# Kernel optimization log

Hardware: AMD Instinct MI355X
Metric: run time of the kernel (lower is better)

## Reference

```python
import jax, jax.numpy as jnp
import numpy as np
import math

WIDTH_POW = 10
WIDTH = 2 ** WIDTH_POW      # 1024
DEPTH = 20
BATCH = 8192
TWO_PI = 2.0 * math.pi


def setup_inputs() -> dict:
    key = jax.random.key(0)
    kx, ka = jax.random.split(key)
    # X is [width, batch] (features-first, matching the torch module's dim-0 padding)
    X = jax.random.normal(kx, (WIDTH, BATCH), dtype=jnp.float32)
    # angles ~ Uniform[0, 2*pi), as in the torch initializer
    angles = jax.random.uniform(ka, (DEPTH, WIDTH // 2), dtype=jnp.float32) * TWO_PI
    return {"X": X, "angles": angles}


def _butterfly_layer(X, ang, stride):
    # X: [width, batch]; ang: [width//2]
    w, b = X.shape
    # Pairs: within each block of 2*stride, element j rotates with element j+stride.
    Xr = X.reshape(w // (2 * stride), 2, stride, b)
    x0 = Xr[:, 0]  # [nblocks, stride, batch]
    x1 = Xr[:, 1]
    c = jnp.cos(ang).reshape(-1, stride, 1)
    s = jnp.sin(ang).reshape(-1, stride, 1)
    y0 = c * x0 + s * x1
    y1 = -s * x0 + c * x1
    return jnp.stack([y0, y1], axis=1).reshape(w, b)


def reference(X, angles):
    width = angles.shape[1] * 2
    width_pow = int(round(math.log2(width)))
    # Pad feature dim up to width (no-op here since X.shape[0] == width)
    pad = width - X.shape[0]
    if pad > 0:
        X = jnp.concatenate([X, jnp.zeros((pad, X.shape[1]), dtype=X.dtype)], axis=0)
    depth = angles.shape[0]
    for i in range(depth):  # small fixed loop over layers (structurally distinct strides)
        stride = 2 ** (i % width_pow)
        X = _butterfly_layer(X, angles[i], stride)
    return X
```

## Files before the change

kernel.cpp:

```cpp
#include <hip/hip_runtime.h>
#include <math.h>


#define NROW   1024
#define BATCH  8192
#define BATCH2 (BATCH / 2)
#define DEPTH  20
#define NANG   512
#define TAB_ELEMS (DEPTH * NANG)
#define TAB_BYTES ((size_t)TAB_ELEMS * 8)

typedef float v2f __attribute__((ext_vector_type(2)));

__device__ __host__ __forceinline__ int rowA(int sub, int i){ return (sub << 5) | i; }
__device__ __host__ __forceinline__ int rowB(int sub, int i){ return sub | (i << 5); }

__global__ void build_tab_kernel(const float* __restrict__ ang,
                                 float2* __restrict__ tab) {
    int idx = blockIdx.x * blockDim.x + threadIdx.x;
    if (idx >= TAB_ELEMS) return;
    int l = idx >> 9;
    int slot = idx & (NANG - 1);
    int sub = slot >> 4, p = slot & 15;
    int m10 = l % 10;
    int sp = m10;
    int SL = 1 << (m10 % 5);
    int i0 = 2 * (p / SL) * SL + p % SL;
    int r = (m10 >= 5) ? rowB(sub, i0) : rowA(sub, i0);
    int a = ((r >> (sp + 1)) << sp) | (r & ((1 << sp) - 1));
    float th = ang[l * NANG + a];
    float sv, cv;
    sincosf(th, &sv, &cv);
    tab[idx] = make_float2(cv, sv);
}

__device__ __forceinline__ void rotp(v2f& a, v2f& b, float cv, float sv) {
    v2f c = {cv, cv}, s = {sv, sv};
    v2f x0 = a, x1 = b;
    a = __builtin_elementwise_fma(c, x0, s * x1);
    b = __builtin_elementwise_fma(-s, x0, c * x1);
}

template<int SL>
__device__ __forceinline__ void layer_tab(v2f y[32],
                                          const float4* __restrict__ q4) {
    #pragma unroll
    for (int v = 0; v < 8; ++v) {
        float4 q = q4[v];
        int p0 = 2 * v, p1 = 2 * v + 1;
        int a0 = 2 * (p0 / SL) * SL + p0 % SL;
        int a1 = 2 * (p1 / SL) * SL + p1 % SL;
        rotp(y[a0], y[a0 + SL], q.x, q.y);
        rotp(y[a1], y[a1 + SL], q.z, q.w);
    }
}

template<int SL, bool PB, int SP>
__device__ __forceinline__ void layer_notab(v2f y[32],
                                            const float* __restrict__ angL,
                                            int sub) {
    #pragma unroll
    for (int p = 0; p < 16; ++p) {
        int i0 = 2 * (p / SL) * SL + p % SL;
        int r = PB ? rowB(sub, i0) : rowA(sub, i0);
        int a = ((r >> (SP + 1)) << SP) | (r & ((1 << SP) - 1));
        float th = angL[a];
        float sv, cv;
        __sincosf(th, &sv, &cv);
        rotp(y[i0], y[i0 + SL], cv, sv);
    }
}

template<bool USE_TAB>
__global__ __launch_bounds__(256) void butterfly_kernel(
        const float* __restrict__ X, const float* __restrict__ ang,
        const float2* __restrict__ tab, float* __restrict__ out) {
    __shared__ v2f lds[8 * 1024];
    int t = threadIdx.x;
    int c = t & 7;
    int sub = t >> 3;
    int bid = blockIdx.x;
    int L = ((bid & 7) << 6) | (bid >> 3);
    int col2 = (L << 3) + c;
    int xr = (c & 7) << 1;
    v2f* base = lds + (c << 10);

    v2f y[32];
    const v2f* Xp = reinterpret_cast<const v2f*>(X) + col2;
    #pragma unroll
    for (int i = 0; i < 32; ++i)
        y[i] = Xp[rowA(sub, i) * BATCH2];

    const float4* tf4 = reinterpret_cast<const float4*>(tab);
    if (USE_TAB) {
        layer_tab<1 >(y, tf4 + 0 * 256 + 8 * sub);
        layer_tab<2 >(y, tf4 + 1 * 256 + 8 * sub);
        layer_tab<4 >(y, tf4 + 2 * 256 + 8 * sub);
        layer_tab<8 >(y, tf4 + 3 * 256 + 8 * sub);
        layer_tab<16>(y, tf4 + 4 * 256 + 8 * sub);
    } else {
        layer_notab<1 ,false,0>(y, ang + 0 * NANG, sub);
        layer_notab<2 ,false,1>(y, ang + 1 * NANG, sub);
        layer_notab<4 ,false,2>(y, ang + 2 * NANG, sub);
        layer_notab<8 ,false,3>(y, ang + 3 * NANG, sub);
        layer_notab<16,false,4>(y, ang + 4 * NANG, sub);
    }
    #pragma unroll
    for (int u = 0; u < 16; ++u)
        *reinterpret_cast<float4*>(&base[((sub << 5) + 2 * u) ^ xr]) =
            make_float4(y[2*u].x, y[2*u].y, y[2*u+1].x, y[2*u+1].y);
    __syncthreads();
    #pragma unroll
    for (int i = 0; i < 32; ++i) y[i] = base[rowB(sub, i) ^ xr];

    if (USE_TAB) {
        layer_tab<1 >(y, tf4 + 5 * 256 + 8 * sub);
        layer_tab<2 >(y, tf4 + 6 * 256 + 8 * sub);
        layer_tab<4 >(y, tf4 + 7 * 256 + 8 * sub);
        layer_tab<8 >(y, tf4 + 8 * 256 + 8 * sub);
        layer_tab<16>(y, tf4 + 9 * 256 + 8 * sub);
    } else {
        layer_notab<1 ,true,5>(y, ang + 5 * NANG, sub);
        layer_notab<2 ,true,6>(y, ang + 6 * NANG, sub);
        layer_notab<4 ,true,7>(y, ang + 7 * NANG, sub);
        layer_notab<8 ,true,8>(y, ang + 8 * NANG, sub);
        layer_notab<16,true,9>(y, ang + 9 * NANG, sub);
    }
    __syncthreads();
    #pragma unroll
    for (int i = 0; i < 32; ++i) base[rowB(sub, i) ^ xr] = y[i];
    __syncthreads();
    #pragma unroll
    for (int u = 0; u < 16; ++u) {
        float4 v = *reinterpret_cast<const float4*>(&base[((sub << 5) + 2 * u) ^ xr]);
        y[2*u].x = v.x; y[2*u].y = v.y; y[2*u+1].x = v.z; y[2*u+1].y = v.w;
    }

    if (USE_TAB) {
        layer_tab<1 >(y, tf4 + 10 * 256 + 8 * sub);
        layer_tab<2 >(y, tf4 + 11 * 256 + 8 * sub);
        layer_tab<4 >(y, tf4 + 12 * 256 + 8 * sub);
        layer_tab<8 >(y, tf4 + 13 * 256 + 8 * sub);
        layer_tab<16>(y, tf4 + 14 * 256 + 8 * sub);
    } else {
        layer_notab<1 ,false,0>(y, ang + 10 * NANG, sub);
        layer_notab<2 ,false,1>(y, ang + 11 * NANG, sub);
        layer_notab<4 ,false,2>(y, ang + 12 * NANG, sub);
        layer_notab<8 ,false,3>(y, ang + 13 * NANG, sub);
        layer_notab<16,false,4>(y, ang + 14 * NANG, sub);
    }
    __syncthreads();
    #pragma unroll
    for (int u = 0; u < 16; ++u)
        *reinterpret_cast<float4*>(&base[((sub << 5) + 2 * u) ^ xr]) =
            make_float4(y[2*u].x, y[2*u].y, y[2*u+1].x, y[2*u+1].y);
    __syncthreads();
    #pragma unroll
    for (int i = 0; i < 32; ++i) y[i] = base[rowB(sub, i) ^ xr];

    if (USE_TAB) {
        layer_tab<1 >(y, tf4 + 15 * 256 + 8 * sub);
        layer_tab<2 >(y, tf4 + 16 * 256 + 8 * sub);
        layer_tab<4 >(y, tf4 + 17 * 256 + 8 * sub);
        layer_tab<8 >(y, tf4 + 18 * 256 + 8 * sub);
        layer_tab<16>(y, tf4 + 19 * 256 + 8 * sub);
    } else {
        layer_notab<1 ,true,5>(y, ang + 15 * NANG, sub);
        layer_notab<2 ,true,6>(y, ang + 16 * NANG, sub);
        layer_notab<4 ,true,7>(y, ang + 17 * NANG, sub);
        layer_notab<8 ,true,8>(y, ang + 18 * NANG, sub);
        layer_notab<16,true,9>(y, ang + 19 * NANG, sub);
    }

    v2f* Op = reinterpret_cast<v2f*>(out) + col2;
    #pragma unroll
    for (int i = 0; i < 32; ++i)
        Op[rowB(sub, i) * BATCH2] = y[i];
}

extern "C" void kernel_launch(void* const* d_in, const int* in_sizes, int n_in,
                              void* d_out, int out_size, void* d_ws, size_t ws_size,
                              hipStream_t stream) {
    (void)in_sizes; (void)n_in; (void)out_size;
    const float* X   = (const float*)d_in[0];
    const float* ang = (const float*)d_in[1];
    float* out = (float*)d_out;

    bool use_tab = (d_ws != nullptr) && (ws_size >= TAB_BYTES);
    if (use_tab) {
        float2* tab = (float2*)d_ws;
        build_tab_kernel<<<(TAB_ELEMS + 255) / 256, 256, 0, stream>>>(ang, tab);
        butterfly_kernel<true><<<512, 256, 0, stream>>>(X, ang, tab, out);
    } else {
        butterfly_kernel<false><<<512, 256, 0, stream>>>(X, ang, nullptr, out);
    }
}
```

Before: 31.60 us.

## Fuse butterfly layer groups into dense 32x32 matrices applied via bf16 MFMA

Each group of five butterfly layers, which acts inside 32-row subspaces, is folded into a dense 32x32 rotation matrix per subspace. The matrices are built in a preprocessing kernel and split into bf16 hi/lo parts. The main kernel applies the four group matrices with bf16 MFMA instructions, keeping intermediates in LDS between groups. The activations X and the intermediate results are rounded to bf16 at every stage, so precision drops well below the fp32 reference, and MFMA matrix products replace the VALU rotation arithmetic.

```diff
diff --git a/kernel.cpp b/kernel.cpp
--- a/kernel.cpp
+++ b/kernel.cpp
@@ -9,8 +9,146 @@
 #define NANG   512
 #define TAB_ELEMS (DEPTH * NANG)
 #define TAB_BYTES ((size_t)TAB_ELEMS * 8)
+#define WS_MFMA_BYTES ((size_t)(4 * 32 * 1024) * 2 * 2)
 
 typedef float v2f __attribute__((ext_vector_type(2)));
+using bf16x8 = __attribute__((ext_vector_type(8))) short;
+using f32x4  = __attribute__((ext_vector_type(4))) float;
+
+__device__ __forceinline__ unsigned short f2b(float f) {
+    union { float f; unsigned int u; } v; v.f = f;
+    unsigned int u = v.u;
+    return (unsigned short)((u + 0x7FFFu + ((u >> 16) & 1u)) >> 16);
+}
+__device__ __forceinline__ float b2f(unsigned short b) {
+    union { unsigned int u; float f; } v; v.u = ((unsigned int)b) << 16;
+    return v.f;
+}
+
+__global__ void build_w_kernel(const float* __restrict__ ang,
+                               unsigned short* __restrict__ whi,
+                               unsigned short* __restrict__ wlo) {
+    int idx = blockIdx.x * blockDim.x + threadIdx.x;
+    if (idx >= 4096) return;
+    int grp = idx >> 10, b = (idx >> 5) & 31, j = idx & 31;
+    float v[32];
+    #pragma unroll
+    for (int i = 0; i < 32; ++i) v[i] = (i == j) ? 1.f : 0.f;
+    #pragma unroll
+    for (int q = 0; q < 5; ++q) {
+        int SL = 1 << q;
+        int sp = (grp & 1) ? q + 5 : q;
+        int l  = grp * 5 + q;
+        int s  = 1 << sp;
+        #pragma unroll
+        for (int p = 0; p < 16; ++p) {
+            int i0 = ((p >> q) << (q + 1)) | (p & (SL - 1));
+            int i1 = i0 + SL;
+            int r0 = (grp & 1) ? ((i0 << 5) | b) : ((b << 5) | i0);
+            int a  = ((r0 >> (sp + 1)) << sp) | (r0 & (s - 1));
+            float th = ang[l * NANG + a];
+            float sv, cv; sincosf(th, &sv, &cv);
+            float x0 = v[i0], x1 = v[i1];
+            v[i0] = cv * x0 + sv * x1;
+            v[i1] = cv * x1 - sv * x0;
+        }
+    }
+    int mat = grp * 32 + b;
+    #pragma unroll
+    for (int i = 0; i < 32; ++i) {
+        unsigned short h = f2b(v[i]);
+        whi[mat * 1024 + i * 32 + j] = h;
+        wlo[mat * 1024 + i * 32 + j] = f2b(v[i] - b2f(h));
+    }
+}
+
+__global__ __launch_bounds__(512) void mfma_kernel(
+        const float* __restrict__ X,
+        const unsigned short* __restrict__ whi,
+        const unsigned short* __restrict__ wlo,
+        float* __restrict__ out) {
+    __shared__ __align__(16) unsigned short sbuf[2][32768];
+    int t  = threadIdx.x;
+    int ln = t & 63;
+    int w  = t >> 6;
+    int bid = blockIdx.x;
+    int L = ((bid & 7) << 5) | (bid >> 3);
+    int col0 = L << 5;
+
+    {
+        int cc = t & 15, sg = (t >> 4) & 1, bb = t >> 5;
+        int col = col0 + sg * 16 + cc;
+        #pragma unroll
+        for (int half = 0; half < 2; ++half) {
+            int rb = bb + 16 * half;
+            int site = rb * 2 + sg;
+            #pragma unroll
+            for (int g = 0; g < 4; ++g) {
+                unsigned int uu[4];
+                #pragma unroll
+                for (int jj = 0; jj < 4; ++jj) {
+                    float va = X[(rb * 32 + g * 8 + 2 * jj) * BATCH + col];
+                    float vb = X[(rb * 32 + g * 8 + 2 * jj + 1) * BATCH + col];
+                    uu[jj] = (unsigned int)f2b(va) | ((unsigned int)f2b(vb) << 16);
+                }
+                *reinterpret_cast<uint4*>(&sbuf[0][site * 512 + g * 128 + cc * 8]) =
+                    make_uint4(uu[0], uu[1], uu[2], uu[3]);
+            }
+        }
+    }
+    __syncthreads();
+
+    const bf16x8* WH = reinterpret_cast<const bf16x8*>(whi);
+    const bf16x8* WL = reinterpret_cast<const bf16x8*>(wlo);
+    int r15 = ln & 15, kg = ln >> 4;
+
+    #pragma unroll
+    for (int grp = 0; grp < 4; ++grp) {
+        int cur = grp & 1;
+        #pragma unroll
+        for (int m = 0; m < 4; ++m) {
+            int rb  = (w & 7) + 8 * m;
+            int mat = grp * 32 + rb;
+            bf16x8 ah0 = WH[mat * 128 + (r15     ) * 4 + kg];
+            bf16x8 ah1 = WH[mat * 128 + (r15 + 16) * 4 + kg];
+            bf16x8 al0 = WL[mat * 128 + (r15     ) * 4 + kg];
+            bf16x8 al1 = WL[mat * 128 + (r15 + 16) * 4 + kg];
+            #pragma unroll
+            for (int sg2 = 0; sg2 < 2; ++sg2) {
+                int site = rb * 2 + sg2;
+                bf16x8 bf = *reinterpret_cast<const bf16x8*>(
+                    &sbuf[cur][site * 512 + kg * 128 + r15 * 8]);
+                f32x4 acc0 = {0.f, 0.f, 0.f, 0.f};
+                f32x4 acc1 = {0.f, 0.f, 0.f, 0.f};
+                acc0 = __builtin_amdgcn_mfma_f32_16x16x32_bf16(ah0, bf, acc0, 0, 0, 0);
+                acc0 = __builtin_amdgcn_mfma_f32_16x16x32_bf16(al0, bf, acc0, 0, 0, 0);
+                acc1 = __builtin_amdgcn_mfma_f32_16x16x32_bf16(ah1, bf, acc1, 0, 0, 0);
+                acc1 = __builtin_amdgcn_mfma_f32_16x16x32_bf16(al1, bf, acc1, 0, 0, 0);
+                if (grp < 3) {
+                    #pragma unroll
+                    for (int e = 0; e < 4; ++e) {
+                        int k0 = kg * 4 + e;
+                        int k1 = 16 + kg * 4 + e;
+                        sbuf[cur ^ 1][(k0 * 2 + sg2) * 512 + (rb >> 3) * 128 +
+                                      r15 * 8 + (rb & 7)] = f2b(acc0[e]);
+                        sbuf[cur ^ 1][(k1 * 2 + sg2) * 512 + (rb >> 3) * 128 +
+                                      r15 * 8 + (rb & 7)] = f2b(acc1[e]);
+                    }
+                } else {
+                    int col = col0 + sg2 * 16 + r15;
+                    #pragma unroll
+                    for (int e = 0; e < 4; ++e) {
+                        int r0 = (kg * 4 + e) * 32 + rb;
+                        int r1 = (16 + kg * 4 + e) * 32 + rb;
+                        out[r0 * BATCH + col] = acc0[e];
+                        out[r1 * BATCH + col] = acc1[e];
+                    }
+                }
+            }
+        }
+        if (grp < 3) __syncthreads();
+    }
+}
 
 __device__ __host__ __forceinline__ int rowA(int sub, int i){ return (sub << 5) | i; }
 __device__ __host__ __forceinline__ int rowB(int sub, int i){ return sub | (i << 5); }
@@ -186,8 +324,12 @@
     const float* ang = (const float*)d_in[1];
     float* out = (float*)d_out;
 
-    bool use_tab = (d_ws != nullptr) && (ws_size >= TAB_BYTES);
-    if (use_tab) {
+    if (d_ws != nullptr && ws_size >= WS_MFMA_BYTES) {
+        unsigned short* whi = (unsigned short*)d_ws;
+        unsigned short* wlo = whi + 4 * 32 * 1024;
+        build_w_kernel<<<16, 256, 0, stream>>>(ang, whi, wlo);
+        mfma_kernel<<<256, 512, 0, stream>>>(X, whi, wlo, out);
+    } else if (d_ws != nullptr && ws_size >= TAB_BYTES) {
         float2* tab = (float2*)d_ws;
         build_tab_kernel<<<(TAB_ELEMS + 255) / 256, 256, 0, stream>>>(ang, tab);
         butterfly_kernel<true><<<512, 256, 0, stream>>>(X, ang, tab, out);
```

New measurement: 62.75 us. 98.6% more time.
